# Optimization experiments

Hardware: AMD Instinct MI355X
Metric: run time of the kernel (lower is better)

The kernel has to match this reference:

```python
import jax, jax.numpy as jnp
import numpy as np


def setup_inputs() -> dict:
    key = jax.random.key(0)
    k1, k2, k3 = jax.random.split(key, 3)
    B, Cin, D, H, W = 16, 3, 16, 128, 128
    Cout, K = 24, 3
    x = jax.random.normal(k1, (B, Cin, D, H, W), dtype=jnp.float32)
    # torch Conv3d default init scale ~ 1/sqrt(fan_in); use small scale for stability
    fan_in = Cin * K * K * K
    conv_weight = jax.random.normal(k2, (Cout, Cin, K, K, K), dtype=jnp.float32) / np.sqrt(fan_in)
    conv_bias = jax.random.normal(k3, (Cout,), dtype=jnp.float32) * 0.01
    return {"x": x, "conv_weight": conv_weight, "conv_bias": conv_bias}


def reference(x, conv_weight, conv_bias):
    # Conv3d, stride=1, padding=0, dilation=1, groups=1
    y = jax.lax.conv_general_dilated(
        x, conv_weight,
        window_strides=(1, 1, 1),
        padding='VALID',
        dimension_numbers=('NCDHW', 'OIDHW', 'NCDHW'),
    )
    y = y + conv_bias[None, :, None, None, None]  # [B, Cout, D', H', W']
    y = jnp.min(y, axis=2)                        # min over depth -> [B, Cout, H', W']
    return jax.nn.softmax(y, axis=1)              # softmax over channels
```

## Files before the change

### kernel.cpp

```cpp
#include <hip/hip_runtime.h>
#include <math.h>

#define CIN 3
#define DIN 16
#define HIN 128
#define WIN 128
#define COUT 24
#define HOUT 126
#define DOUT 14

using f16x8 = __attribute__((ext_vector_type(8))) _Float16;
using f32x4 = __attribute__((ext_vector_type(4))) float;

#define ROWSTRIDE 18
#define SLOT_HALVES (162 * ROWSTRIDE)
#define LDS_HALVES  (4 * SLOT_HALVES + 96)

__global__ __launch_bounds__(256) void conv3d_min_softmax_mfma(
    const float* __restrict__ x,
    const float* __restrict__ wgt,
    const float* __restrict__ bias,
    float* __restrict__ out)
{
    __shared__ _Float16 imX[LDS_HALVES];

    const int tid  = threadIdx.x;
    const int wv   = tid >> 6;
    const int lane = tid & 63;
    const int cl   = lane & 15;
    const int kg   = lane >> 4;

    const int wchunk = blockIdx.x;
    const int band   = blockIdx.y;
    const int b      = blockIdx.z;
    const int w0 = (wchunk < 7) ? wchunk * 16 : 110;
    const int h0 = (band   < 7) ? band   * 16 : 110;

    const float* xb = x + (size_t)b * (CIN * DIN * HIN * WIN);

    for (int i = 3 * SLOT_HALVES + tid; i < LDS_HALVES; i += 256)
        imX[i] = (_Float16)0.f;

    f16x8 bw[3][2];
    #pragma unroll
    for (int kd = 0; kd < 3; ++kd)
      #pragma unroll
      for (int hf = 0; hf < 2; ++hf)
        #pragma unroll
        for (int j = 0; j < 8; ++j) {
          int k  = kg * 8 + j;
          int co = hf * 16 + cl;
          float wvv = 0.f;
          if (k < 27 && co < 24) {
            int kh = k / 9, rem = k - kh * 9, ci = rem / 3, kw = rem - ci * 3;
            wvv = wgt[((co * 3 + ci) * 3 + kd) * 9 + kh * 3 + kw];
          }
          bw[kd][hf][j] = (_Float16)wvv;
        }

    const float bias0 = bias[cl];
    const float bias1 = (cl < 8) ? bias[16 + cl] : 0.f;

    int goff[11];
    int lidx[11];
    int eidx[11];
    #pragma unroll
    for (int it = 0; it < 11; ++it) {
      int e = tid + it * 256;
      eidx[it] = e;
      int ec = (e < 2592) ? e : 0;
      int hrow = ec / 144, e2 = ec - hrow * 144;
      int ci   = e2 / 48,  e3 = e2 - ci * 48;
      int kw   = e3 >> 4,  px = e3 & 15;
      goff[it] = (ci * DIN) * (HIN * WIN) + (h0 + hrow) * WIN + (w0 + kw + px);
      lidx[it] = (hrow * 9 + ci * 3 + kw) * ROWSTRIDE + px;
    }

    #pragma unroll 1
    for (int s = 0; s < 3; ++s) {
      #pragma unroll
      for (int it = 0; it < 11; ++it) {
        if (eidx[it] < 2592) {
          float v = xb[goff[it] + s * (HIN * WIN)];
          imX[s * SLOT_HALVES + lidx[it]] = (_Float16)v;
        }
      }
    }
    __syncthreads();

    float mn[4][2][4];
    #pragma unroll
    for (int t = 0; t < 4; ++t)
      #pragma unroll
      for (int hf = 0; hf < 2; ++hf)
        #pragma unroll
        for (int j = 0; j < 4; ++j) mn[t][hf][j] = 3.4e38f;

    #pragma unroll 1
    for (int dp = 0; dp < DOUT; ++dp) {
      float stash[11];
      const int s = dp + 3;
      const bool doBuild = (s < DIN);
      if (doBuild) {
        #pragma unroll
        for (int it = 0; it < 11; ++it)
          if (eidx[it] < 2592)
            stash[it] = xb[goff[it] + s * (HIN * WIN)];
      }

      #pragma unroll
      for (int t = 0; t < 4; ++t) {
        const int rel_h = wv * 4 + t;
        const int rowbase = (rel_h * 9 + kg * 8) * ROWSTRIDE + cl;

        f16x8 A[3];
        #pragma unroll
        for (int kd = 0; kd < 3; ++kd) {
          const _Float16* ap = &imX[((dp + kd) & 3) * SLOT_HALVES + rowbase];
          #pragma unroll
          for (int j = 0; j < 8; ++j)
            A[kd][j] = ap[j * ROWSTRIDE];
        }

        f32x4 z = {0.f, 0.f, 0.f, 0.f};
        f32x4 acc0 = __builtin_amdgcn_mfma_f32_16x16x32_f16(A[0], bw[0][0], z, 0, 0, 0);
        f32x4 acc1 = __builtin_amdgcn_mfma_f32_16x16x32_f16(A[0], bw[0][1], z, 0, 0, 0);
        acc0 = __builtin_amdgcn_mfma_f32_16x16x32_f16(A[1], bw[1][0], acc0, 0, 0, 0);
        acc1 = __builtin_amdgcn_mfma_f32_16x16x32_f16(A[1], bw[1][1], acc1, 0, 0, 0);
        acc0 = __builtin_amdgcn_mfma_f32_16x16x32_f16(A[2], bw[2][0], acc0, 0, 0, 0);
        acc1 = __builtin_amdgcn_mfma_f32_16x16x32_f16(A[2], bw[2][1], acc1, 0, 0, 0);

        #pragma unroll
        for (int j = 0; j < 4; ++j) {
          mn[t][0][j] = fminf(mn[t][0][j], acc0[j]);
          mn[t][1][j] = fminf(mn[t][1][j], acc1[j]);
        }
      }

      if (doBuild) {
        #pragma unroll
        for (int it = 0; it < 11; ++it)
          if (eidx[it] < 2592)
            imX[(s & 3) * SLOT_HALVES + lidx[it]] = (_Float16)stash[it];
      }
      __syncthreads();
    }

    float* ob = out + (size_t)b * COUT * HOUT * HOUT;
    #pragma unroll
    for (int t = 0; t < 4; ++t) {
      const int h = h0 + wv * 4 + t;
      #pragma unroll
      for (int j = 0; j < 4; ++j) {
        float v0 = mn[t][0][j] + bias0;
        float v1 = (cl < 8) ? (mn[t][1][j] + bias1) : -3.4e38f;
        float mx = fmaxf(v0, v1);
        #pragma unroll
        for (int msk = 1; msk < 16; msk <<= 1)
          mx = fmaxf(mx, __shfl_xor(mx, msk));
        float e0 = __expf(v0 - mx);
        float e1 = (cl < 8) ? __expf(v1 - mx) : 0.f;
        float sm = e0 + e1;
        #pragma unroll
        for (int msk = 1; msk < 16; msk <<= 1)
          sm += __shfl_xor(sm, msk);
        float r = 1.f / sm;
        const int w = w0 + kg * 4 + j;
        ob[((size_t)cl * HOUT + h) * HOUT + w] = e0 * r;
        if (cl < 8)
          ob[((size_t)(16 + cl) * HOUT + h) * HOUT + w] = e1 * r;
      }
    }
}

extern "C" void kernel_launch(void* const* d_in, const int* in_sizes, int n_in,
                              void* d_out, int out_size, void* d_ws, size_t ws_size,
                              hipStream_t stream) {
    const float* x    = (const float*)d_in[0];
    const float* wgt  = (const float*)d_in[1];
    const float* bias = (const float*)d_in[2];
    float* out        = (float*)d_out;

    dim3 grid(8, 8, 16);
    dim3 block(256);
    conv3d_min_softmax_mfma<<<grid, block, 0, stream>>>(x, wgt, bias, out);
}
```

Measured before the change: 82.78 us.

## Store im2col in LDS as pre-packed f16x8 MFMA fragments

The LDS image is now stored in the exact per-lane A-fragment order, so each MFMA operand is one 16-byte LDS read instead of eight strided half loads. Each thread now gathers 32 global values per slice instead of about 11, so the same input is loaded roughly three times over, mostly served by cache. That raises global load instructions and register pressure, which matters because launch bounds now ask for 2 blocks per CU.

```diff
diff --git a/kernel.cpp b/kernel.cpp
--- a/kernel.cpp
+++ b/kernel.cpp
@@ -8,21 +8,18 @@
 #define COUT 24
 #define HOUT 126
 #define DOUT 14
+#define HW (HIN * WIN)
 
 using f16x8 = __attribute__((ext_vector_type(8))) _Float16;
 using f32x4 = __attribute__((ext_vector_type(4))) float;
 
-#define ROWSTRIDE 18
-#define SLOT_HALVES (162 * ROWSTRIDE)
-#define LDS_HALVES  (4 * SLOT_HALVES + 96)
-
-__global__ __launch_bounds__(256) void conv3d_min_softmax_mfma(
+__global__ __launch_bounds__(256, 2) void conv3d_min_softmax_mfma(
     const float* __restrict__ x,
     const float* __restrict__ wgt,
     const float* __restrict__ bias,
     float* __restrict__ out)
 {
-    __shared__ _Float16 imX[LDS_HALVES];
+    __shared__ f16x8 imX[4 * 1024];
 
     const int tid  = threadIdx.x;
     const int wv   = tid >> 6;
@@ -36,10 +33,7 @@
     const int w0 = (wchunk < 7) ? wchunk * 16 : 110;
     const int h0 = (band   < 7) ? band   * 16 : 110;
 
-    const float* xb = x + (size_t)b * (CIN * DIN * HIN * WIN);
-
-    for (int i = 3 * SLOT_HALVES + tid; i < LDS_HALVES; i += 256)
-        imX[i] = (_Float16)0.f;
+    const float* xb = x + (size_t)b * (CIN * DIN * HW);
 
     f16x8 bw[3][2];
     #pragma unroll
@@ -61,29 +55,38 @@
     const float bias0 = bias[cl];
     const float bias1 = (cl < 8) ? bias[16 + cl] : 0.f;
 
-    int goff[11];
-    int lidx[11];
-    int eidx[11];
+    int gof[4][8];
     #pragma unroll
-    for (int it = 0; it < 11; ++it) {
-      int e = tid + it * 256;
-      eidx[it] = e;
-      int ec = (e < 2592) ? e : 0;
-      int hrow = ec / 144, e2 = ec - hrow * 144;
-      int ci   = e2 / 48,  e3 = e2 - ci * 48;
-      int kw   = e3 >> 4,  px = e3 & 15;
-      goff[it] = (ci * DIN) * (HIN * WIN) + (h0 + hrow) * WIN + (w0 + kw + px);
-      lidx[it] = (hrow * 9 + ci * 3 + kw) * ROWSTRIDE + px;
+    for (int it = 0; it < 4; ++it) {
+      const int idx   = tid + it * 256;
+      const int rel_h = idx >> 6;
+      const int tkg   = (idx >> 4) & 3;
+      const int tcl   = idx & 15;
+      #pragma unroll
+      for (int j = 0; j < 8; ++j) {
+        const int k = tkg * 8 + j;
+        int g = -1;
+        if (k < 27) {
+          int kh = k / 9, rem = k - kh * 9, ci = rem / 3, kw = rem - ci * 3;
+          g = ci * (DIN * HW) + (h0 + rel_h + kh) * WIN + (w0 + kw + tcl);
+        }
+        gof[it][j] = g;
+      }
     }
 
     #pragma unroll 1
     for (int s = 0; s < 3; ++s) {
       #pragma unroll
-      for (int it = 0; it < 11; ++it) {
-        if (eidx[it] < 2592) {
-          float v = xb[goff[it] + s * (HIN * WIN)];
-          imX[s * SLOT_HALVES + lidx[it]] = (_Float16)v;
+      for (int it = 0; it < 4; ++it) {
+        f16x8 pk;
+        #pragma unroll
+        for (int j = 0; j < 8; ++j) {
+          const int g = gof[it][j];
+          float v = 0.f;
+          if (g >= 0) v = xb[g + s * HW];
+          pk[j] = (_Float16)v;
         }
+        imX[s * 1024 + tid + it * 256] = pk;
       }
     }
     __syncthreads();
@@ -98,37 +101,36 @@
 
     #pragma unroll 1
     for (int dp = 0; dp < DOUT; ++dp) {
-      float stash[11];
       const int s = dp + 3;
       const bool doBuild = (s < DIN);
+
+      float stv[4][8];
       if (doBuild) {
         #pragma unroll
-        for (int it = 0; it < 11; ++it)
-          if (eidx[it] < 2592)
-            stash[it] = xb[goff[it] + s * (HIN * WIN)];
+        for (int it = 0; it < 4; ++it)
+          #pragma unroll
+          for (int j = 0; j < 8; ++j) {
+            const int g = gof[it][j];
+            stv[it][j] = (g >= 0) ? xb[g + s * HW] : 0.f;
+          }
       }
 
       #pragma unroll
       for (int t = 0; t < 4; ++t) {
         const int rel_h = wv * 4 + t;
-        const int rowbase = (rel_h * 9 + kg * 8) * ROWSTRIDE + cl;
+        const int tb = rel_h * 64 + kg * 16 + cl;
 
-        f16x8 A[3];
-        #pragma unroll
-        for (int kd = 0; kd < 3; ++kd) {
-          const _Float16* ap = &imX[((dp + kd) & 3) * SLOT_HALVES + rowbase];
-          #pragma unroll
-          for (int j = 0; j < 8; ++j)
-            A[kd][j] = ap[j * ROWSTRIDE];
-        }
+        f16x8 A0 = imX[((dp + 0) & 3) * 1024 + tb];
+        f16x8 A1 = imX[((dp + 1) & 3) * 1024 + tb];
+        f16x8 A2 = imX[((dp + 2) & 3) * 1024 + tb];
 
         f32x4 z = {0.f, 0.f, 0.f, 0.f};
-        f32x4 acc0 = __builtin_amdgcn_mfma_f32_16x16x32_f16(A[0], bw[0][0], z, 0, 0, 0);
-        f32x4 acc1 = __builtin_amdgcn_mfma_f32_16x16x32_f16(A[0], bw[0][1], z, 0, 0, 0);
-        acc0 = __builtin_amdgcn_mfma_f32_16x16x32_f16(A[1], bw[1][0], acc0, 0, 0, 0);
-        acc1 = __builtin_amdgcn_mfma_f32_16x16x32_f16(A[1], bw[1][1], acc1, 0, 0, 0);
-        acc0 = __builtin_amdgcn_mfma_f32_16x16x32_f16(A[2], bw[2][0], acc0, 0, 0, 0);
-        acc1 = __builtin_amdgcn_mfma_f32_16x16x32_f16(A[2], bw[2][1], acc1, 0, 0, 0);
+        f32x4 acc0 = __builtin_amdgcn_mfma_f32_16x16x32_f16(A0, bw[0][0], z, 0, 0, 0);
+        f32x4 acc1 = __builtin_amdgcn_mfma_f32_16x16x32_f16(A0, bw[0][1], z, 0, 0, 0);
+        acc0 = __builtin_amdgcn_mfma_f32_16x16x32_f16(A1, bw[1][0], acc0, 0, 0, 0);
+        acc1 = __builtin_amdgcn_mfma_f32_16x16x32_f16(A1, bw[1][1], acc1, 0, 0, 0);
+        acc0 = __builtin_amdgcn_mfma_f32_16x16x32_f16(A2, bw[2][0], acc0, 0, 0, 0);
+        acc1 = __builtin_amdgcn_mfma_f32_16x16x32_f16(A2, bw[2][1], acc1, 0, 0, 0);
 
         #pragma unroll
         for (int j = 0; j < 4; ++j) {
@@ -139,9 +141,12 @@
 
       if (doBuild) {
         #pragma unroll
-        for (int it = 0; it < 11; ++it)
-          if (eidx[it] < 2592)
-            imX[(s & 3) * SLOT_HALVES + lidx[it]] = (_Float16)stash[it];
+        for (int it = 0; it < 4; ++it) {
+          f16x8 pk;
+          #pragma unroll
+          for (int j = 0; j < 8; ++j) pk[j] = (_Float16)stv[it][j];
+          imX[(s & 3) * 1024 + tid + it * 256] = pk;
+        }
       }
       __syncthreads();
     }
```

After: 126.8 us. 53.2% more time.

## Keep depth-slice A fragments in registers and halve LDS ring buffer

Applied to the files above, without the earlier changes.

Rotates the three depth-slice A operand fragments through registers, so each new depth slice is read from LDS once instead of three times per output depth. The LDS ring shrinks from four slots to two and launch bounds request three blocks per CU to raise occupancy. The cost is more VGPRs for 12 f16x8 fragments plus register rotation, and an extra barrier ordering per iteration. Register pressure under the occupancy hint could cause spills.

```diff
diff --git a/kernel.cpp b/kernel.cpp
--- a/kernel.cpp
+++ b/kernel.cpp
@@ -8,15 +8,17 @@
 #define COUT 24
 #define HOUT 126
 #define DOUT 14
+#define HW (HIN * WIN)
 
 using f16x8 = __attribute__((ext_vector_type(8))) _Float16;
 using f32x4 = __attribute__((ext_vector_type(4))) float;
 
 #define ROWSTRIDE 18
 #define SLOT_HALVES (162 * ROWSTRIDE)
-#define LDS_HALVES  (4 * SLOT_HALVES + 96)
-
-__global__ __launch_bounds__(256) void conv3d_min_softmax_mfma(
+#define TAIL 96
+#define LDS_HALVES (2 * SLOT_HALVES + TAIL)
+
+__global__ __launch_bounds__(256, 3) void conv3d_min_softmax_mfma(
     const float* __restrict__ x,
     const float* __restrict__ wgt,
     const float* __restrict__ bias,
@@ -36,9 +38,9 @@
     const int w0 = (wchunk < 7) ? wchunk * 16 : 110;
     const int h0 = (band   < 7) ? band   * 16 : 110;
 
-    const float* xb = x + (size_t)b * (CIN * DIN * HIN * WIN);
-
-    for (int i = 3 * SLOT_HALVES + tid; i < LDS_HALVES; i += 256)
+    const float* xb = x + (size_t)b * (CIN * DIN * HW);
+
+    for (int i = 2 * SLOT_HALVES + tid; i < LDS_HALVES; i += 256)
         imX[i] = (_Float16)0.f;
 
     f16x8 bw[3][2];
@@ -72,21 +74,45 @@
       int hrow = ec / 144, e2 = ec - hrow * 144;
       int ci   = e2 / 48,  e3 = e2 - ci * 48;
       int kw   = e3 >> 4,  px = e3 & 15;
-      goff[it] = (ci * DIN) * (HIN * WIN) + (h0 + hrow) * WIN + (w0 + kw + px);
+      goff[it] = (ci * DIN) * HW + (h0 + hrow) * WIN + (w0 + kw + px);
       lidx[it] = (hrow * 9 + ci * 3 + kw) * ROWSTRIDE + px;
     }
 
+    int rbase[4];
+    #pragma unroll
+    for (int t = 0; t < 4; ++t)
+      rbase[t] = ((wv * 4 + t) * 9 + kg * 8) * ROWSTRIDE + cl;
+
     #pragma unroll 1
-    for (int s = 0; s < 3; ++s) {
-      #pragma unroll
-      for (int it = 0; it < 11; ++it) {
-        if (eidx[it] < 2592) {
-          float v = xb[goff[it] + s * (HIN * WIN)];
-          imX[s * SLOT_HALVES + lidx[it]] = (_Float16)v;
-        }
-      }
+    for (int s = 0; s < 2; ++s) {
+      #pragma unroll
+      for (int it = 0; it < 11; ++it)
+        if (eidx[it] < 2592)
+          imX[s * SLOT_HALVES + lidx[it]] = (_Float16)xb[goff[it] + s * HW];
     }
     __syncthreads();
+
+    f16x8 A0[4], A1[4], A2[4];
+    #pragma unroll
+    for (int t = 0; t < 4; ++t)
+      #pragma unroll
+      for (int j = 0; j < 8; ++j) {
+        A0[t][j] = imX[0 * SLOT_HALVES + rbase[t] + j * ROWSTRIDE];
+        A1[t][j] = imX[1 * SLOT_HALVES + rbase[t] + j * ROWSTRIDE];
+      }
+    __syncthreads();
+
+    #pragma unroll
+    for (int it = 0; it < 11; ++it)
+      if (eidx[it] < 2592)
+        imX[0 * SLOT_HALVES + lidx[it]] = (_Float16)xb[goff[it] + 2 * HW];
+    __syncthreads();
+
+    #pragma unroll
+    for (int t = 0; t < 4; ++t)
+      #pragma unroll
+      for (int j = 0; j < 8; ++j)
+        A2[t][j] = imX[0 * SLOT_HALVES + rbase[t] + j * ROWSTRIDE];
 
     float mn[4][2][4];
     #pragma unroll
@@ -98,38 +124,25 @@
 
     #pragma unroll 1
     for (int dp = 0; dp < DOUT; ++dp) {
+      const bool more = (dp < DOUT - 1);
+
       float stash[11];
-      const int s = dp + 3;
-      const bool doBuild = (s < DIN);
-      if (doBuild) {
+      if (more) {
         #pragma unroll
         for (int it = 0; it < 11; ++it)
           if (eidx[it] < 2592)
-            stash[it] = xb[goff[it] + s * (HIN * WIN)];
+            stash[it] = xb[goff[it] + (dp + 3) * HW];
       }
 
       #pragma unroll
       for (int t = 0; t < 4; ++t) {
-        const int rel_h = wv * 4 + t;
-        const int rowbase = (rel_h * 9 + kg * 8) * ROWSTRIDE + cl;
-
-        f16x8 A[3];
-        #pragma unroll
-        for (int kd = 0; kd < 3; ++kd) {
-          const _Float16* ap = &imX[((dp + kd) & 3) * SLOT_HALVES + rowbase];
-          #pragma unroll
-          for (int j = 0; j < 8; ++j)
-            A[kd][j] = ap[j * ROWSTRIDE];
-        }
-
         f32x4 z = {0.f, 0.f, 0.f, 0.f};
-        f32x4 acc0 = __builtin_amdgcn_mfma_f32_16x16x32_f16(A[0], bw[0][0], z, 0, 0, 0);
-        f32x4 acc1 = __builtin_amdgcn_mfma_f32_16x16x32_f16(A[0], bw[0][1], z, 0, 0, 0);
-        acc0 = __builtin_amdgcn_mfma_f32_16x16x32_f16(A[1], bw[1][0], acc0, 0, 0, 0);
-        acc1 = __builtin_amdgcn_mfma_f32_16x16x32_f16(A[1], bw[1][1], acc1, 0, 0, 0);
-        acc0 = __builtin_amdgcn_mfma_f32_16x16x32_f16(A[2], bw[2][0], acc0, 0, 0, 0);
-        acc1 = __builtin_amdgcn_mfma_f32_16x16x32_f16(A[2], bw[2][1], acc1, 0, 0, 0);
-
+        f32x4 acc0 = __builtin_amdgcn_mfma_f32_16x16x32_f16(A0[t], bw[0][0], z, 0, 0, 0);
+        f32x4 acc1 = __builtin_amdgcn_mfma_f32_16x16x32_f16(A0[t], bw[0][1], z, 0, 0, 0);
+        acc0 = __builtin_amdgcn_mfma_f32_16x16x32_f16(A1[t], bw[1][0], acc0, 0, 0, 0);
+        acc1 = __builtin_amdgcn_mfma_f32_16x16x32_f16(A1[t], bw[1][1], acc1, 0, 0, 0);
+        acc0 = __builtin_amdgcn_mfma_f32_16x16x32_f16(A2[t], bw[2][0], acc0, 0, 0, 0);
+        acc1 = __builtin_amdgcn_mfma_f32_16x16x32_f16(A2[t], bw[2][1], acc1, 0, 0, 0);
         #pragma unroll
         for (int j = 0; j < 4; ++j) {
           mn[t][0][j] = fminf(mn[t][0][j], acc0[j]);
@@ -137,13 +150,21 @@
         }
       }
 
-      if (doBuild) {
+      if (more) {
+        const int sb = ((dp + 1) & 1) * SLOT_HALVES;
         #pragma unroll
         for (int it = 0; it < 11; ++it)
           if (eidx[it] < 2592)
-            imX[(s & 3) * SLOT_HALVES + lidx[it]] = (_Float16)stash[it];
-      }
-      __syncthreads();
+            imX[sb + lidx[it]] = (_Float16)stash[it];
+        __syncthreads();
+        #pragma unroll
+        for (int t = 0; t < 4; ++t) { A0[t] = A1[t]; A1[t] = A2[t]; }
+        #pragma unroll
+        for (int t = 0; t < 4; ++t)
+          #pragma unroll
+          for (int j = 0; j < 8; ++j)
+            A2[t][j] = imX[sb + rbase[t] + j * ROWSTRIDE];
+      }
     }
 
     float* ob = out + (size_t)b * COUT * HOUT * HOUT;
```

After: 176.6 us. +113.4%, slower.
